# Optimization experiments

Measured on AMD Instinct MI355X. Metric: run time of the kernel, lower is better.

## Reference

```python
import jax, jax.numpy as jnp
import numpy as np

UNITS = 2048
D_IN = 96
BATCH = 64
T = 512
C_IN = 10        # connectivity_input: nnz per input-kernel row
C_REC = 10       # connectivity_recurrent: nnz per recurrent-kernel column
INPUT_SCALING = 1.0
SPECTRAL_RADIUS = 0.99
LEAKY = 1.0


def setup_inputs() -> dict:
    rng = np.random.default_rng(0)
    # --- input kernel: sparse (D_IN, UNITS), C_IN nonzeros per row (COO) ---
    krows = np.repeat(np.arange(D_IN), C_IN).astype(np.int32)                 # [D_IN*C_IN]
    kcols = np.stack([rng.choice(UNITS, size=C_IN, replace=False)
                      for _ in range(D_IN)]).reshape(-1).astype(np.int32)
    kvals = (2.0 * (2.0 * rng.random(D_IN * C_IN) - 1.0)).astype(np.float32) * np.float32(INPUT_SCALING)
    # --- recurrent kernel: sparse (UNITS, UNITS), C_REC nonzeros per column ---
    # rec_idx[i, j] = source row feeding output unit (column) i
    rec_idx = np.stack([rng.choice(UNITS, size=C_REC, replace=False)
                        for _ in range(UNITS)]).astype(np.int32)              # [UNITS, C_REC]
    rec_vals = (2.0 * (2.0 * rng.random((UNITS, C_REC)) - 1.0)).astype(np.float32)
    # spectral-radius normalization via exact eigenvalues (matches tf.linalg.eig path, leaky==1)
    W = np.zeros((UNITS, UNITS), np.float32)
    W[rec_idx.reshape(-1), np.repeat(np.arange(UNITS), C_REC)] = rec_vals.reshape(-1)
    rho = np.abs(np.linalg.eigvals(W)).max()
    rec_vals = rec_vals * np.float32(SPECTRAL_RADIUS / rho)
    # --- bias ---
    bias = (2.0 * rng.random(UNITS) - 1.0).astype(np.float32) * np.float32(INPUT_SCALING)
    key = jax.random.key(0)
    inputs = jax.random.normal(key, (BATCH, T, D_IN), dtype=jnp.float32)
    state0 = jnp.zeros((BATCH, UNITS), dtype=jnp.float32)
    return {
        "inputs": inputs,
        "state0": state0,
        "kernel_vals": jnp.asarray(kvals),
        "rec_vals": jnp.asarray(rec_vals),
        "bias": jnp.asarray(bias),
        "kernel_rows": jnp.asarray(krows),
        "kernel_cols": jnp.asarray(kcols),
        "rec_idx": jnp.asarray(rec_idx),
    }


def reference(inputs, state0, kernel_vals, rec_vals, bias, kernel_rows, kernel_cols, rec_idx):
    units = bias.shape[0]

    def step(h, x_t):                                     # h: [B, units], x_t: [B, D_IN]
        # input_part = x_t @ kernel (sparse COO, fixed degree per row)
        contrib = x_t[:, kernel_rows] * kernel_vals       # [B, nnz_in]
        input_part = jax.ops.segment_sum(contrib.T, kernel_cols, num_segments=units).T  # [B, units]
        # state_part = h @ W (fixed C_REC sources per output unit -> gather+reduce)
        state_part = jnp.einsum('bnc,nc->bn', h[:, rec_idx], rec_vals)  # [B, units]
        h_new = h * (1.0 - LEAKY) + jnp.tanh(input_part + bias + state_part) * LEAKY
        return h_new, h_new

    _, ys = jax.lax.scan(step, state0, jnp.swapaxes(inputs, 0, 1))  # ys: [T, B, units]
    return jnp.swapaxes(ys, 0, 1)                                   # [B, T, units]
```

## Files before the change

### kernel.cpp

```cpp
#include <hip/hip_runtime.h>

namespace {
constexpr int UNITS = 2048;
constexpr int D_IN  = 96;
constexpr int BATCH = 64;
constexpr int T     = 512;
constexpr int NNZ   = 960;
constexpr int C_REC = 10;
constexpr int CHUNK = 128;
constexpr int NT    = 1024;

constexpr int HA = 0;
constexpr int HB = 8192;
constexpr int IA = 16384;
constexpr int IB = 24576;
constexpr int XO = 32768;
constexpr int LDS_BYTES = XO + CHUNK * D_IN * 4;
}

typedef float f32x2 __attribute__((ext_vector_type(2)));

__device__ __forceinline__ void bar_lds() {
  asm volatile("s_waitcnt lgkmcnt(0)\n\ts_barrier" ::: "memory");
}

__device__ __forceinline__ float fast_tanh(float x) {
  float e = __expf(2.0f * x);
  return 1.0f - __fdividef(2.0f, e + 1.0f);
}

#define STEP(HC, HN, IR, IW, SLOT_NEXT, DO_SCATTER, TSTEP)                     \
  {                                                                            \
    if ((DO_SCATTER) && tid < NNZ) {                                           \
      float xv = *(const float*)(smem + XO + (SLOT_NEXT) * (D_IN * 4) + krb);  \
      atomicAdd((float*)(smem + (IW) + kcb), xv * kv);                         \
    }                                                                          \
    f32x2 in2 = *(f32x2*)(smem + (IR) + tid * 8);                              \
    *(f32x2*)(smem + (IR) + tid * 8) = (f32x2){0.f, 0.f};                      \
    float s0 = in2.x + bias2.x;                                                \
    float s1 = in2.y + bias2.y;                                                \
    _Pragma("unroll")                                                          \
    for (int c = 0; c < C_REC; ++c) {                                          \
      s0 += *(const float*)(smem + (HC) + idxb0[c]) * w0[c];                   \
      s1 += *(const float*)(smem + (HC) + idxb1[c]) * w1[c];                   \
    }                                                                          \
    f32x2 hh = {fast_tanh(s0), fast_tanh(s1)};                                 \
    *(f32x2*)(smem + (HN) + tid * 8) = hh;                                     \
    __builtin_nontemporal_store(hh, outp + (size_t)(TSTEP) * (UNITS / 2));     \
    bar_lds();                                                                 \
  }

__global__ __launch_bounds__(NT, 4) void reservoir_kernel(
    const float* __restrict__ inputs, const float* __restrict__ state0,
    const float* __restrict__ kvals,  const float* __restrict__ rvals,
    const float* __restrict__ bias,   const int* __restrict__ krows,
    const int* __restrict__ kcols,    const int* __restrict__ ridx,
    float* __restrict__ out)
{
  __shared__ __align__(16) char smem[LDS_BYTES];
  const int tid = threadIdx.x;
  const int b   = blockIdx.x;
  const int u0  = tid * 2;

  *(float4*)(smem + IA + tid * 16) = make_float4(0.f, 0.f, 0.f, 0.f);
  *(f32x2*)(smem + HA + tid * 8) = *(const f32x2*)(state0 + b * UNITS + u0);

  int   idxb0[C_REC], idxb1[C_REC];
  float w0[C_REC], w1[C_REC];
#pragma unroll
  for (int c = 0; c < C_REC; ++c) {
    idxb0[c] = ridx[u0 * C_REC + c] * 4;
    idxb1[c] = ridx[u0 * C_REC + C_REC + c] * 4;
    w0[c]    = rvals[u0 * C_REC + c];
    w1[c]    = rvals[u0 * C_REC + C_REC + c];
  }
  const f32x2 bias2 = *(const f32x2*)(bias + u0);

  int krb = 0, kcb = 0; float kv = 0.f;
  if (tid < NNZ) {
    krb = krows[tid] * 4;
    kcb = kcols[tid] * 4;
    kv  = kvals[tid];
  }

  const float* xin  = inputs + (size_t)b * (T * D_IN);
  f32x2*       outp = (f32x2*)out + (size_t)b * (T * (UNITS / 2)) + tid;

  __syncthreads();

  for (int tb = 0; tb < T; tb += CHUNK) {
#pragma unroll
    for (int k = 0; k < 3; ++k) {
      float4 v = *(const float4*)(xin + tb * D_IN + (tid + k * NT) * 4);
      *(float4*)(smem + XO + (tid + k * NT) * 16) = v;
    }
    bar_lds();
    if (tid < NNZ) {
      float xv = *(const float*)(smem + XO + krb);
      atomicAdd((float*)(smem + IA + kcb), xv * kv);
    }
    bar_lds();
#pragma unroll 1
    for (int ts = 0; ts < CHUNK; ts += 2) {
      STEP(HA, HB, IA, IB, ts + 1, true,              tb + ts);
      STEP(HB, HA, IB, IA, ts + 2, (ts + 2) < CHUNK,  tb + ts + 1);
    }
  }
}

extern "C" void kernel_launch(void* const* d_in, const int* in_sizes, int n_in,
                              void* d_out, int out_size, void* d_ws, size_t ws_size,
                              hipStream_t stream) {
  const float* inputs = (const float*)d_in[0];
  const float* state0 = (const float*)d_in[1];
  const float* kvals  = (const float*)d_in[2];
  const float* rvals  = (const float*)d_in[3];
  const float* bias   = (const float*)d_in[4];
  const int*   krows  = (const int*)d_in[5];
  const int*   kcols  = (const int*)d_in[6];
  const int*   ridx   = (const int*)d_in[7];

  reservoir_kernel<<<dim3(BATCH), dim3(NT), 0, stream>>>(
      inputs, state0, kvals, rvals, bias, krows, kcols, ridx, (float*)d_out);
}
```

Before: 1.263 ms.

## Halve threads to four units each and bank-aware reorder recurrent gathers

```diff
diff --git a/kernel.cpp b/kernel.cpp
--- a/kernel.cpp
+++ b/kernel.cpp
@@ -8,7 +8,7 @@
 constexpr int NNZ   = 960;
 constexpr int C_REC = 10;
 constexpr int CHUNK = 128;
-constexpr int NT    = 1024;
+constexpr int NT    = 512;
 
 constexpr int HA = 0;
 constexpr int HB = 8192;
@@ -16,9 +16,13 @@
 constexpr int IB = 24576;
 constexpr int XO = 32768;
 constexpr int LDS_BYTES = XO + CHUNK * D_IN * 4;
+
+constexpr int IDXP_BYTES = 4 * C_REC * NT * 4;
+constexpr int PERM_BYTES = 2 * IDXP_BYTES;
 }
 
 typedef float f32x2 __attribute__((ext_vector_type(2)));
+typedef float f32x4 __attribute__((ext_vector_type(4)));
 
 __device__ __forceinline__ void bar_lds() {
   asm volatile("s_waitcnt lgkmcnt(0)\n\ts_barrier" ::: "memory");
@@ -29,75 +33,120 @@
   return 1.0f - __fdividef(2.0f, e + 1.0f);
 }
 
+__global__ void prep_kernel(const int* __restrict__ ridx,
+                            const float* __restrict__ rvals,
+                            int* __restrict__ idxp, float* __restrict__ wp) {
+  const int tid  = threadIdx.x;
+  const int lane = tid & 63;
+  const int phi  = (lane * C_REC) >> 6;
+  for (int lu = 0; lu < 4; ++lu) {
+    const int u = tid * 4 + lu;
+    int idx[C_REC]; float w[C_REC];
+    for (int c = 0; c < C_REC; ++c) {
+      idx[c] = ridx[u * C_REC + c];
+      w[c]   = rvals[u * C_REC + c];
+    }
+    for (int i = 1; i < C_REC; ++i) {
+      int ii = idx[i]; float ww = w[i]; int bi = ii & 31;
+      int j = i - 1;
+      while (j >= 0 && (idx[j] & 31) > bi) { idx[j+1] = idx[j]; w[j+1] = w[j]; --j; }
+      idx[j+1] = ii; w[j+1] = ww;
+    }
+    for (int q = 0; q < C_REC; ++q) {
+      int s = q - phi; if (s < 0) s += C_REC;
+      idxp[(lu * C_REC + s) * NT + tid] = idx[q] * 4;
+      wp  [(lu * C_REC + s) * NT + tid] = w[q];
+    }
+  }
+}
+
+#define RDECL(L, lu, n)                                                        \
+  const int   i##L##n = PERM ? idxp[((lu) * C_REC + (n)) * NT + tid]           \
+                             : ridx[(u0 + (lu)) * C_REC + (n)] * 4;            \
+  const float w##L##n = PERM ? wp[((lu) * C_REC + (n)) * NT + tid]             \
+                             : rvals[(u0 + (lu)) * C_REC + (n)];
+#define RDECL10(L, lu)                                                         \
+  RDECL(L, lu, 0) RDECL(L, lu, 1) RDECL(L, lu, 2) RDECL(L, lu, 3)              \
+  RDECL(L, lu, 4) RDECL(L, lu, 5) RDECL(L, lu, 6) RDECL(L, lu, 7)              \
+  RDECL(L, lu, 8) RDECL(L, lu, 9)
+
+#define GAT(HC, L, n)                                                          \
+  s##L += *(const float*)(smem + (HC) + i##L##n) * w##L##n;
+#define GAT10(HC, L)                                                           \
+  GAT(HC, L, 0) GAT(HC, L, 1) GAT(HC, L, 2) GAT(HC, L, 3) GAT(HC, L, 4)        \
+  GAT(HC, L, 5) GAT(HC, L, 6) GAT(HC, L, 7) GAT(HC, L, 8) GAT(HC, L, 9)
+
 #define STEP(HC, HN, IR, IW, SLOT_NEXT, DO_SCATTER, TSTEP)                     \
   {                                                                            \
-    if ((DO_SCATTER) && tid < NNZ) {                                           \
-      float xv = *(const float*)(smem + XO + (SLOT_NEXT) * (D_IN * 4) + krb);  \
-      atomicAdd((float*)(smem + (IW) + kcb), xv * kv);                         \
+    if (DO_SCATTER) {                                                          \
+      float xv1 = *(const float*)(smem + XO + (SLOT_NEXT) * (D_IN * 4) + krb1);\
+      atomicAdd((float*)(smem + (IW) + kcb1), xv1 * kv1);                      \
+      if (tid < NNZ - NT) {                                                    \
+        float xv2 = *(const float*)(smem + XO + (SLOT_NEXT)*(D_IN*4) + krb2);  \
+        atomicAdd((float*)(smem + (IW) + kcb2), xv2 * kv2);                    \
+      }                                                                        \
     }                                                                          \
-    f32x2 in2 = *(f32x2*)(smem + (IR) + tid * 8);                              \
-    *(f32x2*)(smem + (IR) + tid * 8) = (f32x2){0.f, 0.f};                      \
-    float s0 = in2.x + bias2.x;                                                \
-    float s1 = in2.y + bias2.y;                                                \
-    _Pragma("unroll")                                                          \
-    for (int c = 0; c < C_REC; ++c) {                                          \
-      s0 += *(const float*)(smem + (HC) + idxb0[c]) * w0[c];                   \
-      s1 += *(const float*)(smem + (HC) + idxb1[c]) * w1[c];                   \
-    }                                                                          \
-    f32x2 hh = {fast_tanh(s0), fast_tanh(s1)};                                 \
-    *(f32x2*)(smem + (HN) + tid * 8) = hh;                                     \
-    __builtin_nontemporal_store(hh, outp + (size_t)(TSTEP) * (UNITS / 2));     \
+    f32x4 in4 = *(f32x4*)(smem + (IR) + tid * 16);                             \
+    *(f32x4*)(smem + (IR) + tid * 16) = (f32x4){0.f, 0.f, 0.f, 0.f};           \
+    float sa = in4.x + bias4.x, sb = in4.y + bias4.y;                          \
+    float sc = in4.z + bias4.z, sd = in4.w + bias4.w;                          \
+    GAT10(HC, a) GAT10(HC, b) GAT10(HC, c) GAT10(HC, d)                        \
+    f32x4 hh = {fast_tanh(sa), fast_tanh(sb), fast_tanh(sc), fast_tanh(sd)};   \
+    *(f32x4*)(smem + (HN) + tid * 16) = hh;                                    \
+    __builtin_nontemporal_store(hh, outp + (size_t)(TSTEP) * (UNITS / 4));     \
     bar_lds();                                                                 \
   }
 
-__global__ __launch_bounds__(NT, 4) void reservoir_kernel(
+template <bool PERM>
+__global__ __launch_bounds__(NT, 2) void reservoir_kernel(
     const float* __restrict__ inputs, const float* __restrict__ state0,
     const float* __restrict__ kvals,  const float* __restrict__ rvals,
     const float* __restrict__ bias,   const int* __restrict__ krows,
     const int* __restrict__ kcols,    const int* __restrict__ ridx,
+    const int* __restrict__ idxp,     const float* __restrict__ wp,
     float* __restrict__ out)
 {
   __shared__ __align__(16) char smem[LDS_BYTES];
   const int tid = threadIdx.x;
   const int b   = blockIdx.x;
-  const int u0  = tid * 2;
+  const int u0  = tid * 4;
 
-  *(float4*)(smem + IA + tid * 16) = make_float4(0.f, 0.f, 0.f, 0.f);
-  *(f32x2*)(smem + HA + tid * 8) = *(const f32x2*)(state0 + b * UNITS + u0);
+  *(f32x4*)(smem + IA + tid * 16) = (f32x4){0.f, 0.f, 0.f, 0.f};
+  *(f32x4*)(smem + IB + tid * 16) = (f32x4){0.f, 0.f, 0.f, 0.f};
+  *(f32x4*)(smem + HA + tid * 16) = *(const f32x4*)(state0 + b * UNITS + u0);
 
-  int   idxb0[C_REC], idxb1[C_REC];
-  float w0[C_REC], w1[C_REC];
-#pragma unroll
-  for (int c = 0; c < C_REC; ++c) {
-    idxb0[c] = ridx[u0 * C_REC + c] * 4;
-    idxb1[c] = ridx[u0 * C_REC + C_REC + c] * 4;
-    w0[c]    = rvals[u0 * C_REC + c];
-    w1[c]    = rvals[u0 * C_REC + C_REC + c];
-  }
-  const f32x2 bias2 = *(const f32x2*)(bias + u0);
+  RDECL10(a, 0) RDECL10(b, 1) RDECL10(c, 2) RDECL10(d, 3)
 
-  int krb = 0, kcb = 0; float kv = 0.f;
-  if (tid < NNZ) {
-    krb = krows[tid] * 4;
-    kcb = kcols[tid] * 4;
-    kv  = kvals[tid];
+  const f32x4 bias4 = *(const f32x4*)(bias + u0);
+
+  int krb1 = krows[tid] * 4, kcb1 = kcols[tid] * 4;
+  float kv1 = kvals[tid];
+  int krb2 = 0, kcb2 = 0; float kv2 = 0.f;
+  if (tid < NNZ - NT) {
+    krb2 = krows[NT + tid] * 4;
+    kcb2 = kcols[NT + tid] * 4;
+    kv2  = kvals[NT + tid];
   }
 
   const float* xin  = inputs + (size_t)b * (T * D_IN);
-  f32x2*       outp = (f32x2*)out + (size_t)b * (T * (UNITS / 2)) + tid;
+  f32x4*       outp = (f32x4*)out + (size_t)b * (T * (UNITS / 4)) + tid;
 
   __syncthreads();
 
   for (int tb = 0; tb < T; tb += CHUNK) {
 #pragma unroll
-    for (int k = 0; k < 3; ++k) {
+    for (int k = 0; k < 6; ++k) {
       float4 v = *(const float4*)(xin + tb * D_IN + (tid + k * NT) * 4);
       *(float4*)(smem + XO + (tid + k * NT) * 16) = v;
     }
     bar_lds();
-    if (tid < NNZ) {
-      float xv = *(const float*)(smem + XO + krb);
-      atomicAdd((float*)(smem + IA + kcb), xv * kv);
+    {
+      float xv1 = *(const float*)(smem + XO + krb1);
+      atomicAdd((float*)(smem + IA + kcb1), xv1 * kv1);
+      if (tid < NNZ - NT) {
+        float xv2 = *(const float*)(smem + XO + krb2);
+        atomicAdd((float*)(smem + IA + kcb2), xv2 * kv2);
+      }
     }
     bar_lds();
 #pragma unroll 1
@@ -120,6 +169,17 @@
   const int*   kcols  = (const int*)d_in[6];
   const int*   ridx   = (const int*)d_in[7];
 
-  reservoir_kernel<<<dim3(BATCH), dim3(NT), 0, stream>>>(
-      inputs, state0, kvals, rvals, bias, krows, kcols, ridx, (float*)d_out);
+  int*   idxp = (int*)d_ws;
+  float* wp   = (float*)((char*)d_ws + IDXP_BYTES);
+
+  if (ws_size >= (size_t)PERM_BYTES) {
+    prep_kernel<<<dim3(1), dim3(NT), 0, stream>>>(ridx, rvals, idxp, wp);
+    reservoir_kernel<true><<<dim3(BATCH), dim3(NT), 0, stream>>>(
+        inputs, state0, kvals, rvals, bias, krows, kcols, ridx, idxp, wp,
+        (float*)d_out);
+  } else {
+    reservoir_kernel<false><<<dim3(BATCH), dim3(NT), 0, stream>>>(
+        inputs, state0, kvals, rvals, bias, krows, kcols, ridx, idxp, wp,
+        (float*)d_out);
+  }
 }
```

New measurement: 1.398 ms. +10.7%, slower.

## Duplicate state into swizzled LDS copy and schedule gathers to avoid bank conflicts

Applied to the files above, without the earlier changes.

```diff
diff --git a/kernel.cpp b/kernel.cpp
--- a/kernel.cpp
+++ b/kernel.cpp
@@ -10,12 +10,18 @@
 constexpr int CHUNK = 128;
 constexpr int NT    = 1024;
 
-constexpr int HA = 0;
-constexpr int HB = 8192;
-constexpr int IA = 16384;
-constexpr int IB = 24576;
-constexpr int XO = 32768;
+constexpr int HPING = 0;
+constexpr int HPONG = 16384;
+constexpr int IA    = 32768;
+constexpr int IB    = 40960;
+constexpr int XO    = 49152;
 constexpr int LDS_BYTES = XO + CHUNK * D_IN * 4;
+
+constexpr int OFFA_OFS = 0;
+constexpr int WA_OFS   = C_REC * NT * 4;
+constexpr int OFFB_OFS = 2 * C_REC * NT * 4;
+constexpr int WB_OFS   = 3 * C_REC * NT * 4;
+constexpr int WS_NEED  = 4 * C_REC * NT * 4;
 }
 
 typedef float f32x2 __attribute__((ext_vector_type(2)));
@@ -28,6 +34,68 @@
   float e = __expf(2.0f * x);
   return 1.0f - __fdividef(2.0f, e + 1.0f);
 }
+
+__global__ __launch_bounds__(1024) void prep_kernel(
+    const int* __restrict__ ridx, const float* __restrict__ rvals,
+    int* __restrict__ offA, float* __restrict__ wA,
+    int* __restrict__ offB, float* __restrict__ wB)
+{
+  __shared__ unsigned short off16[UNITS][C_REC][2];
+  __shared__ unsigned char  hist[16][20][32];
+  __shared__ unsigned short rem[16][64][2];
+  const int tid = threadIdx.x;
+
+  for (int i = tid; i < UNITS * C_REC; i += 1024) {
+    int idx = ridx[i];
+    int v   = idx ^ ((idx >> 5) & 31);
+    off16[i / C_REC][i % C_REC][0] = (unsigned short)(idx * 4);
+    off16[i / C_REC][i % C_REC][1] = (unsigned short)(8192 + v * 4);
+  }
+  for (int i = tid; i < 16 * 20 * 32; i += 1024) ((unsigned char*)hist)[i] = 0;
+  for (int i = tid; i < 16 * 64 * 2; i += 1024) ((unsigned short*)rem)[i] = 0x3FF;
+  __syncthreads();
+
+  const int w = tid >> 6, l = tid & 63;
+  for (int step = 0; step < 20 + 63; ++step) {
+    const int s = step - l;
+    if (s >= 0 && s < 20) {
+      const int usel = s & 1;
+      const int ord  = s >> 1;
+      const int u    = 2 * (w * 64 + l) + usel;
+      unsigned m = rem[w][l][usel];
+      int beste = 0, bestload = 255, bestoff = 0;
+#pragma unroll
+      for (int e = 0; e < C_REC; ++e) {
+        if (!((m >> e) & 1)) continue;
+#pragma unroll
+        for (int c = 0; c < 2; ++c) {
+          int off = off16[u][e][c];
+          int ld  = hist[w][s][(off >> 2) & 31];
+          if (ld < bestload) { bestload = ld; beste = e; bestoff = off; }
+        }
+      }
+      hist[w][s][(bestoff >> 2) & 31] = (unsigned char)(bestload + 1);
+      rem[w][l][usel] = (unsigned short)(m & ~(1u << beste));
+      const int tmain = w * 64 + l;
+      const float wv  = rvals[u * C_REC + beste];
+      if (usel == 0) { offA[ord * NT + tmain] = bestoff; wA[ord * NT + tmain] = wv; }
+      else           { offB[ord * NT + tmain] = bestoff; wB[ord * NT + tmain] = wv; }
+    }
+    __syncthreads();
+  }
+}
+
+#define RDECL(n)                                                               \
+  const int   oa##n = PERM ? offA[(n) * NT + tid] : ridx[u0 * C_REC + (n)] * 4;\
+  const float va##n = PERM ? wA[(n) * NT + tid]   : rvals[u0 * C_REC + (n)];   \
+  const int   ob##n = PERM ? offB[(n) * NT + tid]                              \
+                           : ridx[(u0 + 1) * C_REC + (n)] * 4;                 \
+  const float vb##n = PERM ? wB[(n) * NT + tid]                                \
+                           : rvals[(u0 + 1) * C_REC + (n)];
+
+#define GAT(HC, n)                                                             \
+  s0 += *(const float*)(smem + (HC) + oa##n) * va##n;                          \
+  s1 += *(const float*)(smem + (HC) + ob##n) * vb##n;
 
 #define STEP(HC, HN, IR, IW, SLOT_NEXT, DO_SCATTER, TSTEP)                     \
   {                                                                            \
@@ -39,22 +107,24 @@
     *(f32x2*)(smem + (IR) + tid * 8) = (f32x2){0.f, 0.f};                      \
     float s0 = in2.x + bias2.x;                                                \
     float s1 = in2.y + bias2.y;                                                \
-    _Pragma("unroll")                                                          \
-    for (int c = 0; c < C_REC; ++c) {                                          \
-      s0 += *(const float*)(smem + (HC) + idxb0[c]) * w0[c];                   \
-      s1 += *(const float*)(smem + (HC) + idxb1[c]) * w1[c];                   \
-    }                                                                          \
+    GAT(HC, 0) GAT(HC, 1) GAT(HC, 2) GAT(HC, 3) GAT(HC, 4)                     \
+    GAT(HC, 5) GAT(HC, 6) GAT(HC, 7) GAT(HC, 8) GAT(HC, 9)                     \
     f32x2 hh = {fast_tanh(s0), fast_tanh(s1)};                                 \
     *(f32x2*)(smem + (HN) + tid * 8) = hh;                                     \
+    f32x2 hb2 = vswap ? (f32x2){hh.y, hh.x} : hh;                              \
+    *(f32x2*)(smem + (HN) + vbyte) = hb2;                                      \
     __builtin_nontemporal_store(hh, outp + (size_t)(TSTEP) * (UNITS / 2));     \
     bar_lds();                                                                 \
   }
 
+template <bool PERM>
 __global__ __launch_bounds__(NT, 4) void reservoir_kernel(
     const float* __restrict__ inputs, const float* __restrict__ state0,
     const float* __restrict__ kvals,  const float* __restrict__ rvals,
     const float* __restrict__ bias,   const int* __restrict__ krows,
     const int* __restrict__ kcols,    const int* __restrict__ ridx,
+    const int* __restrict__ offA,     const float* __restrict__ wA,
+    const int* __restrict__ offB,     const float* __restrict__ wB,
     float* __restrict__ out)
 {
   __shared__ __align__(16) char smem[LDS_BYTES];
@@ -62,18 +132,21 @@
   const int b   = blockIdx.x;
   const int u0  = tid * 2;
 
-  *(float4*)(smem + IA + tid * 16) = make_float4(0.f, 0.f, 0.f, 0.f);
-  *(f32x2*)(smem + HA + tid * 8) = *(const f32x2*)(state0 + b * UNITS + u0);
-
-  int   idxb0[C_REC], idxb1[C_REC];
-  float w0[C_REC], w1[C_REC];
-#pragma unroll
-  for (int c = 0; c < C_REC; ++c) {
-    idxb0[c] = ridx[u0 * C_REC + c] * 4;
-    idxb1[c] = ridx[u0 * C_REC + C_REC + c] * 4;
-    w0[c]    = rvals[u0 * C_REC + c];
-    w1[c]    = rvals[u0 * C_REC + C_REC + c];
-  }
+  const int  v0    = u0 ^ ((u0 >> 5) & 31);
+  const int  vbyte = 8192 + (v0 & ~1) * 4;
+  const bool vswap = (v0 & 1) != 0;
+
+  *(f32x2*)(smem + IA + tid * 8) = (f32x2){0.f, 0.f};
+  *(f32x2*)(smem + IB + tid * 8) = (f32x2){0.f, 0.f};
+
+  f32x2 h0 = *(const f32x2*)(state0 + b * UNITS + u0);
+  *(f32x2*)(smem + HPING + tid * 8) = h0;
+  f32x2 h0b = vswap ? (f32x2){h0.y, h0.x} : h0;
+  *(f32x2*)(smem + HPING + vbyte) = h0b;
+
+  RDECL(0) RDECL(1) RDECL(2) RDECL(3) RDECL(4)
+  RDECL(5) RDECL(6) RDECL(7) RDECL(8) RDECL(9)
+
   const f32x2 bias2 = *(const f32x2*)(bias + u0);
 
   int krb = 0, kcb = 0; float kv = 0.f;
@@ -102,8 +175,8 @@
     bar_lds();
 #pragma unroll 1
     for (int ts = 0; ts < CHUNK; ts += 2) {
-      STEP(HA, HB, IA, IB, ts + 1, true,              tb + ts);
-      STEP(HB, HA, IB, IA, ts + 2, (ts + 2) < CHUNK,  tb + ts + 1);
+      STEP(HPING, HPONG, IA, IB, ts + 1, true,              tb + ts);
+      STEP(HPONG, HPING, IB, IA, ts + 2, (ts + 2) < CHUNK,  tb + ts + 1);
     }
   }
 }
@@ -120,6 +193,19 @@
   const int*   kcols  = (const int*)d_in[6];
   const int*   ridx   = (const int*)d_in[7];
 
-  reservoir_kernel<<<dim3(BATCH), dim3(NT), 0, stream>>>(
-      inputs, state0, kvals, rvals, bias, krows, kcols, ridx, (float*)d_out);
-}
+  int*   offA = (int*)((char*)d_ws + OFFA_OFS);
+  float* wA   = (float*)((char*)d_ws + WA_OFS);
+  int*   offB = (int*)((char*)d_ws + OFFB_OFS);
+  float* wB   = (float*)((char*)d_ws + WB_OFS);
+
+  if (ws_size >= (size_t)WS_NEED) {
+    prep_kernel<<<dim3(1), dim3(1024), 0, stream>>>(ridx, rvals, offA, wA, offB, wB);
+    reservoir_kernel<true><<<dim3(BATCH), dim3(NT), 0, stream>>>(
+        inputs, state0, kvals, rvals, bias, krows, kcols, ridx,
+        offA, wA, offB, wB, (float*)d_out);
+  } else {
+    reservoir_kernel<false><<<dim3(BATCH), dim3(NT), 0, stream>>>(
+        inputs, state0, kvals, rvals, bias, krows, kcols, ridx,
+        offA, wA, offB, wB, (float*)d_out);
+  }
+}
```

After: 1.214 ms. 1.04x faster.

## Process two batch rows per block with interleaved state and bank-aware gather schedule

Applied to the files above, without the earlier changes.

```diff
diff --git a/kernel.cpp b/kernel.cpp
--- a/kernel.cpp
+++ b/kernel.cpp
@@ -7,18 +7,21 @@
 constexpr int T     = 512;
 constexpr int NNZ   = 960;
 constexpr int C_REC = 10;
-constexpr int CHUNK = 128;
 constexpr int NT    = 1024;
 
 constexpr int HA = 0;
-constexpr int HB = 8192;
-constexpr int IA = 16384;
-constexpr int IB = 24576;
-constexpr int XO = 32768;
-constexpr int LDS_BYTES = XO + CHUNK * D_IN * 4;
+constexpr int HB = 16384;
+constexpr int IA = 32768;
+constexpr int IB = 49152;
+constexpr int LDS_BYTES = 65536;
+
+constexpr int OFFS_OFS = 0;
+constexpr int WTAB_OFS = 20 * NT * 4;
+constexpr int WS_NEED  = 40 * NT * 4;
 }
 
 typedef float f32x2 __attribute__((ext_vector_type(2)));
+typedef float f32x4 __attribute__((ext_vector_type(4)));
 
 __device__ __forceinline__ void bar_lds() {
   asm volatile("s_waitcnt lgkmcnt(0)\n\ts_barrier" ::: "memory");
@@ -29,82 +32,131 @@
   return 1.0f - __fdividef(2.0f, e + 1.0f);
 }
 
-#define STEP(HC, HN, IR, IW, SLOT_NEXT, DO_SCATTER, TSTEP)                     \
+__global__ __launch_bounds__(64) void prep_sched(
+    const int* __restrict__ ridx, const float* __restrict__ rvals,
+    int* __restrict__ offs, float* __restrict__ wtab)
+{
+  const int w = blockIdx.x, l = threadIdx.x;
+  __shared__ unsigned char hist[20][16];
+  if (l < 16)
+    for (int s = 0; s < 20; ++s) hist[s][l] = 0;
+  __syncthreads();
+  const int tidm = w * 64 + l;
+  const int uA = 2 * tidm, uB = uA + 1;
+  unsigned remA = 0x3FF, remB = 0x3FF;
+  for (int step = 0; step < 20 + 63; ++step) {
+    const int s = step - l;
+    if (s >= 0 && s < 20) {
+      const int u = (s & 1) ? uB : uA;
+      unsigned& rem = (s & 1) ? remB : remA;
+      int beste = 0, bestload = 999, bestidx = 0;
+      for (int e = 0; e < C_REC; ++e) {
+        if (!((rem >> e) & 1)) continue;
+        int idx = ridx[u * C_REC + e];
+        int ld  = hist[s][idx & 15];
+        if (ld < bestload) { bestload = ld; beste = e; bestidx = idx; }
+      }
+      hist[s][bestidx & 15] = (unsigned char)(bestload + 1);
+      rem &= ~(1u << beste);
+      offs[s * NT + tidm] = bestidx * 8;
+      wtab[s * NT + tidm] = rvals[u * C_REC + beste];
+    }
+    __syncthreads();
+  }
+}
+
+#define RDECL(k)                                                               \
+  const int   oA##k = PERM ? offs[(2*(k)) * NT + tid]                          \
+                           : ridx[u0 * C_REC + (k)] * 8;                       \
+  const float wA##k = PERM ? wtab[(2*(k)) * NT + tid]                          \
+                           : rvals[u0 * C_REC + (k)];                          \
+  const int   oB##k = PERM ? offs[(2*(k)+1) * NT + tid]                        \
+                           : ridx[(u0 + 1) * C_REC + (k)] * 8;                 \
+  const float wB##k = PERM ? wtab[(2*(k)+1) * NT + tid]                        \
+                           : rvals[(u0 + 1) * C_REC + (k)];
+
+#define GAT(HC, k)                                                             \
+  { f32x2 ga = *(const f32x2*)(smem + (HC) + oA##k);                           \
+    s0a += ga.x * wA##k; s0b += ga.y * wA##k;                                  \
+    f32x2 gb = *(const f32x2*)(smem + (HC) + oB##k);                           \
+    s1a += gb.x * wB##k; s1b += gb.y * wB##k; }
+
+#define STEP(HC, HN, IR, IW, DO_SCATTER, TSTEP)                                \
   {                                                                            \
-    if ((DO_SCATTER) && tid < NNZ) {                                           \
-      float xv = *(const float*)(smem + XO + (SLOT_NEXT) * (D_IN * 4) + krb);  \
-      atomicAdd((float*)(smem + (IW) + kcb), xv * kv);                         \
+    f32x4 in4 = *(f32x4*)(smem + (IR) + tid * 16);                             \
+    *(f32x4*)(smem + (IR) + tid * 16) = (f32x4){0.f, 0.f, 0.f, 0.f};           \
+    float s0a = in4.x + bias2.x, s0b = in4.y + bias2.x;                        \
+    float s1a = in4.z + bias2.y, s1b = in4.w + bias2.y;                        \
+    GAT(HC, 0) GAT(HC, 1) GAT(HC, 2) GAT(HC, 3) GAT(HC, 4)                     \
+    GAT(HC, 5) GAT(HC, 6) GAT(HC, 7) GAT(HC, 8) GAT(HC, 9)                     \
+    if ((DO_SCATTER) && e0) {                                                  \
+      atomicAdd((float*)(smem + (IW) + kcb),     xa * kv);                     \
+      atomicAdd((float*)(smem + (IW) + kcb + 4), xb * kv);                     \
     }                                                                          \
-    f32x2 in2 = *(f32x2*)(smem + (IR) + tid * 8);                              \
-    *(f32x2*)(smem + (IR) + tid * 8) = (f32x2){0.f, 0.f};                      \
-    float s0 = in2.x + bias2.x;                                                \
-    float s1 = in2.y + bias2.y;                                                \
-    _Pragma("unroll")                                                          \
-    for (int c = 0; c < C_REC; ++c) {                                          \
-      s0 += *(const float*)(smem + (HC) + idxb0[c]) * w0[c];                   \
-      s1 += *(const float*)(smem + (HC) + idxb1[c]) * w1[c];                   \
+    f32x4 hh = {fast_tanh(s0a), fast_tanh(s0b),                                \
+                fast_tanh(s1a), fast_tanh(s1b)};                               \
+    *(f32x4*)(smem + (HN) + tid * 16) = hh;                                    \
+    __builtin_nontemporal_store((f32x2){hh.x, hh.z},                           \
+                                out0 + (size_t)(TSTEP) * (UNITS / 2));         \
+    __builtin_nontemporal_store((f32x2){hh.y, hh.w},                           \
+                                out1 + (size_t)(TSTEP) * (UNITS / 2));         \
+    if (e0) {                                                                  \
+      int tnx = (TSTEP) + 2 < T ? (TSTEP) + 2 : T - 1;                         \
+      xa = xin0[tnx * D_IN + r0];                                              \
+      xb = xin1[tnx * D_IN + r0];                                              \
     }                                                                          \
-    f32x2 hh = {fast_tanh(s0), fast_tanh(s1)};                                 \
-    *(f32x2*)(smem + (HN) + tid * 8) = hh;                                     \
-    __builtin_nontemporal_store(hh, outp + (size_t)(TSTEP) * (UNITS / 2));     \
     bar_lds();                                                                 \
   }
 
-__global__ __launch_bounds__(NT, 4) void reservoir_kernel(
+template <bool PERM>
+__global__ __launch_bounds__(NT, 4) void reservoir2(
     const float* __restrict__ inputs, const float* __restrict__ state0,
     const float* __restrict__ kvals,  const float* __restrict__ rvals,
     const float* __restrict__ bias,   const int* __restrict__ krows,
     const int* __restrict__ kcols,    const int* __restrict__ ridx,
+    const int* __restrict__ offs,     const float* __restrict__ wtab,
     float* __restrict__ out)
 {
   __shared__ __align__(16) char smem[LDS_BYTES];
   const int tid = threadIdx.x;
-  const int b   = blockIdx.x;
-  const int u0  = tid * 2;
+  const int b0  = 2 * blockIdx.x, b1 = b0 + 1;
+  const int u0  = 2 * tid;
 
-  *(float4*)(smem + IA + tid * 16) = make_float4(0.f, 0.f, 0.f, 0.f);
-  *(f32x2*)(smem + HA + tid * 8) = *(const f32x2*)(state0 + b * UNITS + u0);
+  *(f32x4*)(smem + IA + tid * 16) = (f32x4){0.f, 0.f, 0.f, 0.f};
+  *(f32x4*)(smem + IB + tid * 16) = (f32x4){0.f, 0.f, 0.f, 0.f};
+  f32x2 h0a = *(const f32x2*)(state0 + b0 * UNITS + u0);
+  f32x2 h0b = *(const f32x2*)(state0 + b1 * UNITS + u0);
+  *(f32x4*)(smem + HA + tid * 16) = (f32x4){h0a.x, h0b.x, h0a.y, h0b.y};
 
-  int   idxb0[C_REC], idxb1[C_REC];
-  float w0[C_REC], w1[C_REC];
-#pragma unroll
-  for (int c = 0; c < C_REC; ++c) {
-    idxb0[c] = ridx[u0 * C_REC + c] * 4;
-    idxb1[c] = ridx[u0 * C_REC + C_REC + c] * 4;
-    w0[c]    = rvals[u0 * C_REC + c];
-    w1[c]    = rvals[u0 * C_REC + C_REC + c];
-  }
+  RDECL(0) RDECL(1) RDECL(2) RDECL(3) RDECL(4)
+  RDECL(5) RDECL(6) RDECL(7) RDECL(8) RDECL(9)
+
   const f32x2 bias2 = *(const f32x2*)(bias + u0);
 
-  int krb = 0, kcb = 0; float kv = 0.f;
-  if (tid < NNZ) {
-    krb = krows[tid] * 4;
-    kcb = kcols[tid] * 4;
-    kv  = kvals[tid];
+  const bool e0 = tid < NNZ;
+  const int   r0  = e0 ? krows[tid] : 0;
+  const int   kcb = e0 ? kcols[tid] * 8 : 0;
+  const float kv  = e0 ? kvals[tid] : 0.f;
+
+  const float* xin0 = inputs + (size_t)b0 * (T * D_IN);
+  const float* xin1 = inputs + (size_t)b1 * (T * D_IN);
+  f32x2* out0 = (f32x2*)out + (size_t)b0 * (T * (UNITS / 2)) + tid;
+  f32x2* out1 = (f32x2*)out + (size_t)b1 * (T * (UNITS / 2)) + tid;
+
+  float xa = e0 ? xin0[r0] : 0.f;
+  float xb = e0 ? xin1[r0] : 0.f;
+  __syncthreads();
+  if (e0) {
+    atomicAdd((float*)(smem + IA + kcb),     xa * kv);
+    atomicAdd((float*)(smem + IA + kcb + 4), xb * kv);
   }
+  if (e0) { xa = xin0[D_IN + r0]; xb = xin1[D_IN + r0]; }
+  bar_lds();
 
-  const float* xin  = inputs + (size_t)b * (T * D_IN);
-  f32x2*       outp = (f32x2*)out + (size_t)b * (T * (UNITS / 2)) + tid;
-
-  __syncthreads();
-
-  for (int tb = 0; tb < T; tb += CHUNK) {
-#pragma unroll
-    for (int k = 0; k < 3; ++k) {
-      float4 v = *(const float4*)(xin + tb * D_IN + (tid + k * NT) * 4);
-      *(float4*)(smem + XO + (tid + k * NT) * 16) = v;
-    }
-    bar_lds();
-    if (tid < NNZ) {
-      float xv = *(const float*)(smem + XO + krb);
-      atomicAdd((float*)(smem + IA + kcb), xv * kv);
-    }
-    bar_lds();
 #pragma unroll 1
-    for (int ts = 0; ts < CHUNK; ts += 2) {
-      STEP(HA, HB, IA, IB, ts + 1, true,              tb + ts);
-      STEP(HB, HA, IB, IA, ts + 2, (ts + 2) < CHUNK,  tb + ts + 1);
-    }
+  for (int ts = 0; ts < T; ts += 2) {
+    STEP(HA, HB, IA, IB, true,         ts);
+    STEP(HB, HA, IB, IA, (ts + 2) < T, ts + 1);
   }
 }
 
@@ -120,6 +172,17 @@
   const int*   kcols  = (const int*)d_in[6];
   const int*   ridx   = (const int*)d_in[7];
 
-  reservoir_kernel<<<dim3(BATCH), dim3(NT), 0, stream>>>(
-      inputs, state0, kvals, rvals, bias, krows, kcols, ridx, (float*)d_out);
+  int*   offs = (int*)((char*)d_ws + OFFS_OFS);
+  float* wtab = (float*)((char*)d_ws + WTAB_OFS);
+
+  if (ws_size >= (size_t)WS_NEED) {
+    prep_sched<<<dim3(16), dim3(64), 0, stream>>>(ridx, rvals, offs, wtab);
+    reservoir2<true><<<dim3(BATCH / 2), dim3(NT), 0, stream>>>(
+        inputs, state0, kvals, rvals, bias, krows, kcols, ridx, offs, wtab,
+        (float*)d_out);
+  } else {
+    reservoir2<false><<<dim3(BATCH / 2), dim3(NT), 0, stream>>>(
+        inputs, state0, kvals, rvals, bias, krows, kcols, ridx, offs, wtab,
+        (float*)d_out);
+  }
 }
```

Measured after the change: 1.906 ms. 51.0% more time.
